# Optimization experiments

Hardware: AMD Instinct MI355X
Metric: run time of the kernel (lower is better)

The kernel has to match this reference:

```python
import jax, jax.numpy as jnp
import numpy as np
from jax import lax

SR = 4096.0        # sample_rate_Hz
N_LAYERS = 4
N_STATE = 64       # state_dim
E = 2              # d_inner (expand=2, d_model=1)
K = 4              # depthwise conv kernel
DT_RANK = 1
B, L = 32, 4096


def setup_inputs() -> dict:
    key = jax.random.key(0)
    ks = jax.random.split(key, 10)
    s = 0.02
    x = jax.random.normal(ks[0], (B, L), dtype=jnp.float32)
    W_in   = jax.random.normal(ks[1], (N_LAYERS, 1, 2 * E), jnp.float32) * 1.0
    conv_w = jax.random.normal(ks[2], (N_LAYERS, E, K), jnp.float32) * 0.5
    conv_b = jnp.zeros((N_LAYERS, E), jnp.float32)
    W_x    = jax.random.normal(ks[3], (N_LAYERS, E, DT_RANK + 2 * N_STATE), jnp.float32) * s
    W_dt   = jax.random.normal(ks[4], (N_LAYERS, DT_RANK, E), jnp.float32) * s
    b_dt   = jnp.zeros((N_LAYERS, E), jnp.float32)
    # S4D-real style init: A = -exp(A_log), A_log = log(1..N)
    A_log  = jnp.broadcast_to(jnp.log(jnp.arange(1, N_STATE + 1, dtype=jnp.float32)), (N_LAYERS, E, N_STATE)).copy()
    D_skip = jnp.ones((N_LAYERS, E), jnp.float32)
    W_out  = jax.random.normal(ks[5], (N_LAYERS, E, 1), jnp.float32) * s
    return {"x": x, "W_in": W_in, "conv_w": conv_w, "conv_b": conv_b, "W_x": W_x,
            "W_dt": W_dt, "b_dt": b_dt, "A_log": A_log, "D_skip": D_skip, "W_out": W_out}


def _causal_dwconv(u, w, b):
    # u: [B,L,E], w: [E,K] depthwise causal conv
    Klen = w.shape[1]
    up = jnp.pad(u, ((0, 0), (Klen - 1, 0), (0, 0)))
    y = sum(up[:, k:k + u.shape[1], :] * w[None, None, :, k] for k in range(Klen))
    return y + b


def _selective_scan(u, delta, A, Bm, Cm, Dv):
    # u,delta: [B,L,E]; A: [E,N]; Bm,Cm: [B,L,N]; Dv: [E]
    dA = jnp.exp(delta[..., None] * A)                       # [B,L,E,N]
    dBu = delta[..., None] * Bm[:, :, None, :] * u[..., None]  # [B,L,E,N]

    def step(h, inp):
        dA_t, dBu_t, C_t = inp                               # [B,E,N],[B,E,N],[B,N]
        h = dA_t * h + dBu_t
        y = jnp.einsum('ben,bn->be', h, C_t)
        return h, y

    h0 = jnp.zeros((u.shape[0],) + A.shape, dtype=u.dtype)
    _, ys = lax.scan(step, h0, (dA.transpose(1, 0, 2, 3), dBu.transpose(1, 0, 2, 3), Cm.transpose(1, 0, 2)))
    return ys.transpose(1, 0, 2) + u * Dv                    # [B,L,E]


def _mamba_block(x, W_in, conv_w, conv_b, W_x, W_dt, b_dt, A_log, D_skip, W_out):
    # x: [B,L,1]
    xz = x @ W_in                                            # [B,L,2E]
    u, z = xz[..., :E], xz[..., E:]
    u = jax.nn.silu(_causal_dwconv(u, conv_w, conv_b))       # [B,L,E]
    proj = u @ W_x                                           # [B,L,DT_RANK+2N]
    dt = proj[..., :DT_RANK]
    Bm = proj[..., DT_RANK:DT_RANK + N_STATE]
    Cm = proj[..., DT_RANK + N_STATE:]
    delta = jax.nn.softplus(dt @ W_dt + b_dt) / SR           # [B,L,E], timestep tied to sample rate
    A = -jnp.exp(A_log)                                      # [E,N]
    y = _selective_scan(u, delta, A, Bm, Cm, D_skip)
    y = y * jax.nn.silu(z)
    return y @ W_out + x                                     # residual, [B,L,1]


def reference(x, W_in, conv_w, conv_b, W_x, W_dt, b_dt, A_log, D_skip, W_out):
    h = x[..., None]                                         # [B,L,1]
    for i in range(N_LAYERS):
        h = _mamba_block(h, W_in[i], conv_w[i], conv_b[i], W_x[i], W_dt[i],
                         b_dt[i], A_log[i], D_skip[i], W_out[i])
    return h[..., 0]
```

## Files before the change

kernel.cpp:

```cpp
#include <hip/hip_runtime.h>
#include <hip/hip_bf16.h>


constexpr int   Bsz = 32;
constexpr int   Lsz = 4096;
constexpr int   NC  = 32;
constexpr int   CL  = 128;
constexpr float SRinv = 1.0f / 4096.0f;

__device__ __forceinline__ float sigmoidf_(float v) {
    return 1.0f / (1.0f + __expf(-v));
}

__global__ __launch_bounds__(128) void k_chunk_scan(
    const float* __restrict__ xin,
    const float* __restrict__ W_in,
    const float* __restrict__ conv_w,
    const float* __restrict__ conv_b,
    const float* __restrict__ W_x,
    const float* __restrict__ W_dt,
    const float* __restrict__ b_dt,
    const float* __restrict__ A_log,
    float4* __restrict__ ud,
    float*  __restrict__ Pc,
    float*  __restrict__ Sc)
{
    const int c = blockIdx.x, b = blockIdx.y, tid = threadIdx.x;
    __shared__ float  xs[CL + 3];
    __shared__ float4 s_ud[CL];
    const int base = b * Lsz + c * CL;

    for (int i = tid; i < CL + 3; i += 128) {
        int l = c * CL + i - 3;
        xs[i] = (l >= 0) ? xin[b * Lsz + l] : 0.0f;
    }
    __syncthreads();

    {
        const int t = tid;
        float x0 = xs[t], x1 = xs[t + 1], x2 = xs[t + 2], x3 = xs[t + 3];
        float u[2];
        #pragma unroll
        for (int e = 0; e < 2; e++) {
            float v = W_in[e] * (x0 * conv_w[e * 4 + 0] + x1 * conv_w[e * 4 + 1] +
                                 x2 * conv_w[e * 4 + 2] + x3 * conv_w[e * 4 + 3]) +
                      conv_b[e];
            u[e] = v * sigmoidf_(v);
        }
        float dt = u[0] * W_x[0] + u[1] * W_x[129];
        float dl[2];
        #pragma unroll
        for (int e = 0; e < 2; e++) {
            float a = dt * W_dt[e] + b_dt[e];
            float sp = (a > 20.0f) ? a : log1pf(__expf(a));
            dl[e] = sp * SRinv;
        }
        float4 v4 = make_float4(u[0], u[1], dl[0], dl[1]);
        s_ud[t] = v4;
        ud[base + t] = v4;
    }
    __syncthreads();

    const int e = tid >> 6, n = tid & 63;
    const float Aen = -__expf(A_log[e * 64 + n]);
    const float wb0 = W_x[1 + n], wb1 = W_x[129 + 1 + n];
    float P = 1.0f, S = 0.0f;
    #pragma unroll 8
    for (int l = 0; l < CL; l++) {
        float4 v = s_ud[l];
        float ue = e ? v.y : v.x;
        float d  = e ? v.w : v.z;
        float Bn = v.x * wb0 + v.y * wb1;
        float dA = __expf(d * Aen);
        S = dA * S + (d * ue) * Bn;
        P *= dA;
    }
    const int idx = (b * NC + c) * 128 + tid;
    Pc[idx] = P;
    Sc[idx] = S;
}

__global__ __launch_bounds__(256) void k_combine(
    const float* __restrict__ Pc, const float* __restrict__ Sc,
    float* __restrict__ Hinit)
{
    const int idx = blockIdx.x * 256 + threadIdx.x;
    const int b = idx >> 7, en = idx & 127;
    float h = 0.0f;
    #pragma unroll
    for (int c = 0; c < NC; c++) {
        int o = (b * NC + c) * 128 + en;
        Hinit[o] = h;
        h = Pc[o] * h + Sc[o];
    }
}

__global__ __launch_bounds__(128) void k_output(
    const float* __restrict__ xin,
    const float4* __restrict__ ud,
    const float* __restrict__ Hinit,
    const float* __restrict__ W_in,
    const float* __restrict__ W_x,
    const float* __restrict__ A_log,
    const float* __restrict__ D_skip,
    const float* __restrict__ W_out,
    float* __restrict__ out)
{
    const int c = blockIdx.x, b = blockIdx.y, tid = threadIdx.x;
    constexpr int T = 64;
    __shared__ float4 s_ud[CL];
    __shared__ float  xs[CL];
    __shared__ float  ps[128 * 65];
    __shared__ float  ys[T * 2];
    const int base = b * Lsz + c * CL;

    s_ud[tid] = ud[base + tid];
    xs[tid]   = xin[base + tid];

    const int e = tid >> 6, n = tid & 63;
    const float Aen = -__expf(A_log[e * 64 + n]);
    const float wb0 = W_x[1 + n],  wb1 = W_x[129 + 1 + n];
    const float wc0 = W_x[65 + n], wc1 = W_x[129 + 65 + n];
    float h = Hinit[(b * NC + c) * 128 + tid];
    const float wz0 = W_in[2], wz1 = W_in[3];
    const float D0 = D_skip[0], D1 = D_skip[1];
    const float wo0 = W_out[0], wo1 = W_out[1];
    __syncthreads();

    for (int tile = 0; tile < CL / T; tile++) {
        #pragma unroll 8
        for (int t = 0; t < T; t++) {
            float4 v = s_ud[tile * T + t];
            float ue = e ? v.y : v.x;
            float d  = e ? v.w : v.z;
            float Bn = v.x * wb0 + v.y * wb1;
            float Cn = v.x * wc0 + v.y * wc1;
            float dA = __expf(d * Aen);
            h = dA * h + (d * ue) * Bn;
            ps[(t * 2 + e) * 65 + n] = h * Cn;
        }
        __syncthreads();
        {
            const int r = tid, t = r >> 1, re = r & 1;
            const float* row = &ps[r * 65];
            float a0 = 0, a1 = 0, a2 = 0, a3 = 0;
            #pragma unroll
            for (int j = 0; j < 64; j += 4) {
                a0 += row[j]; a1 += row[j + 1]; a2 += row[j + 2]; a3 += row[j + 3];
            }
            float4 v = s_ud[tile * T + t];
            float ue = re ? v.y : v.x;
            ys[r] = (a0 + a1) + (a2 + a3) + ue * (re ? D1 : D0);
        }
        __syncthreads();
        if (tid < T) {
            int l = tile * T + tid;
            float y0 = ys[tid * 2], y1 = ys[tid * 2 + 1];
            float xv = xs[l];
            float z0 = xv * wz0, z1 = xv * wz1;
            out[base + l] = y0 * (z0 * sigmoidf_(z0)) * wo0 +
                            y1 * (z1 * sigmoidf_(z1)) * wo1 + xv;
        }
        __syncthreads();
    }
}

extern "C" void kernel_launch(void* const* d_in, const int* in_sizes, int n_in,
                              void* d_out, int out_size, void* d_ws, size_t ws_size,
                              hipStream_t stream) {
    const float* x      = (const float*)d_in[0];
    const float* W_in   = (const float*)d_in[1];
    const float* conv_w = (const float*)d_in[2];
    const float* conv_b = (const float*)d_in[3];
    const float* W_x    = (const float*)d_in[4];
    const float* W_dt   = (const float*)d_in[5];
    const float* b_dt   = (const float*)d_in[6];
    const float* A_log  = (const float*)d_in[7];
    const float* D_skip = (const float*)d_in[8];
    const float* W_out  = (const float*)d_in[9];
    float* out = (float*)d_out;

    float* ws   = (float*)d_ws;
    float4* ud  = (float4*)ws;
    float* Pc   = ws + (size_t)Bsz * Lsz * 4;
    float* Sc   = Pc + (size_t)Bsz * NC * 128;
    float* Hi   = Sc + (size_t)Bsz * NC * 128;
    float* buf0 = Hi + (size_t)Bsz * NC * 128;
    float* buf1 = buf0 + (size_t)Bsz * Lsz;

    const float* cur = x;
    for (int i = 0; i < 4; i++) {
        float* o = (i == 3) ? out : ((i & 1) ? buf1 : buf0);
        k_chunk_scan<<<dim3(NC, Bsz), 128, 0, stream>>>(
            cur, W_in + i * 4, conv_w + i * 8, conv_b + i * 2,
            W_x + i * 258, W_dt + i * 2, b_dt + i * 2, A_log + i * 128,
            ud, Pc, Sc);
        k_combine<<<16, 256, 0, stream>>>(Pc, Sc, Hi);
        k_output<<<dim3(NC, Bsz), 128, 0, stream>>>(
            cur, ud, Hi, W_in + i * 4, W_x + i * 258,
            A_log + i * 128, D_skip + i * 2, W_out + i * 2, o);
        cur = o;
    }
}
```

Measured before the change: 161.8 us.

## Fold chunk combine into output kernel and halve chunk length

Removes the separate combine kernel: each output block recomputes its starting state by serially folding the packed (P,S) pairs of all preceding chunks. Chunk length drops from 128 to 64 (twice the blocks, shorter serial scans), the per-direction branches are split by e to avoid selects, and the partial-sum reduction is split across two threads per row. This cuts one launch per layer and shortens the dependent chains. In exchange, later chunks perform up to 63 dependent global loads to rebuild their initial state, and the last chunk skips the P/S scan.

New measurement: 214.9 us. +32.8%, slower.

```diff
diff --git a/kernel.cpp b/kernel.cpp
--- a/kernel.cpp
+++ b/kernel.cpp
@@ -4,15 +4,16 @@
 
 constexpr int   Bsz = 32;
 constexpr int   Lsz = 4096;
-constexpr int   NC  = 32;
-constexpr int   CL  = 128;
+constexpr int   NC  = 64;
+constexpr int   CL  = 64;
+constexpr int   T   = 32;
 constexpr float SRinv = 1.0f / 4096.0f;
 
 __device__ __forceinline__ float sigmoidf_(float v) {
     return 1.0f / (1.0f + __expf(-v));
 }
 
-__global__ __launch_bounds__(128) void k_chunk_scan(
+__global__ __launch_bounds__(128) void k_scanA(
     const float* __restrict__ xin,
     const float* __restrict__ W_in,
     const float* __restrict__ conv_w,
@@ -22,8 +23,7 @@
     const float* __restrict__ b_dt,
     const float* __restrict__ A_log,
     float4* __restrict__ ud,
-    float*  __restrict__ Pc,
-    float*  __restrict__ Sc)
+    float2* __restrict__ PS)
 {
     const int c = blockIdx.x, b = blockIdx.y, tid = threadIdx.x;
     __shared__ float  xs[CL + 3];
@@ -36,7 +36,7 @@
     }
     __syncthreads();
 
-    {
+    if (tid < CL) {
         const int t = tid;
         float x0 = xs[t], x1 = xs[t + 1], x2 = xs[t + 2], x3 = xs[t + 3];
         float u[2];
@@ -61,44 +61,38 @@
     }
     __syncthreads();
 
+    if (c == NC - 1) return;
+
     const int e = tid >> 6, n = tid & 63;
     const float Aen = -__expf(A_log[e * 64 + n]);
     const float wb0 = W_x[1 + n], wb1 = W_x[129 + 1 + n];
     float P = 1.0f, S = 0.0f;
-    #pragma unroll 8
-    for (int l = 0; l < CL; l++) {
-        float4 v = s_ud[l];
-        float ue = e ? v.y : v.x;
-        float d  = e ? v.w : v.z;
-        float Bn = v.x * wb0 + v.y * wb1;
-        float dA = __expf(d * Aen);
-        S = dA * S + (d * ue) * Bn;
-        P *= dA;
-    }
-    const int idx = (b * NC + c) * 128 + tid;
-    Pc[idx] = P;
-    Sc[idx] = S;
-}
-
-__global__ __launch_bounds__(256) void k_combine(
-    const float* __restrict__ Pc, const float* __restrict__ Sc,
-    float* __restrict__ Hinit)
-{
-    const int idx = blockIdx.x * 256 + threadIdx.x;
-    const int b = idx >> 7, en = idx & 127;
-    float h = 0.0f;
-    #pragma unroll
-    for (int c = 0; c < NC; c++) {
-        int o = (b * NC + c) * 128 + en;
-        Hinit[o] = h;
-        h = Pc[o] * h + Sc[o];
-    }
-}
-
-__global__ __launch_bounds__(128) void k_output(
+    if (e == 0) {
+        #pragma unroll 8
+        for (int l = 0; l < CL; l++) {
+            float4 v = s_ud[l];
+            float Bn = v.x * wb0 + v.y * wb1;
+            float dA = __expf(v.z * Aen);
+            S = dA * S + (v.z * v.x) * Bn;
+            P *= dA;
+        }
+    } else {
+        #pragma unroll 8
+        for (int l = 0; l < CL; l++) {
+            float4 v = s_ud[l];
+            float Bn = v.x * wb0 + v.y * wb1;
+            float dA = __expf(v.w * Aen);
+            S = dA * S + (v.w * v.y) * Bn;
+            P *= dA;
+        }
+    }
+    PS[(b * NC + c) * 128 + tid] = make_float2(P, S);
+}
+
+__global__ __launch_bounds__(128) void k_scanB(
     const float* __restrict__ xin,
     const float4* __restrict__ ud,
-    const float* __restrict__ Hinit,
+    const float2* __restrict__ PS,
     const float* __restrict__ W_in,
     const float* __restrict__ W_x,
     const float* __restrict__ A_log,
@@ -107,55 +101,74 @@
     float* __restrict__ out)
 {
     const int c = blockIdx.x, b = blockIdx.y, tid = threadIdx.x;
-    constexpr int T = 64;
     __shared__ float4 s_ud[CL];
     __shared__ float  xs[CL];
-    __shared__ float  ps[128 * 65];
-    __shared__ float  ys[T * 2];
+    __shared__ float  ps[T * 2 * 65];
+    __shared__ float  pp[128];
     const int base = b * Lsz + c * CL;
 
-    s_ud[tid] = ud[base + tid];
-    xs[tid]   = xin[base + tid];
+    if (tid < CL) {
+        s_ud[tid] = ud[base + tid];
+        xs[tid]   = xin[base + tid];
+    }
+
+    float h = 0.0f;
+    {
+        const float2* p = &PS[(size_t)b * NC * 128 + tid];
+        for (int cp = 0; cp < c; cp++) {
+            float2 v = p[cp * 128];
+            h = v.x * h + v.y;
+        }
+    }
 
     const int e = tid >> 6, n = tid & 63;
     const float Aen = -__expf(A_log[e * 64 + n]);
     const float wb0 = W_x[1 + n],  wb1 = W_x[129 + 1 + n];
     const float wc0 = W_x[65 + n], wc1 = W_x[129 + 65 + n];
-    float h = Hinit[(b * NC + c) * 128 + tid];
     const float wz0 = W_in[2], wz1 = W_in[3];
     const float D0 = D_skip[0], D1 = D_skip[1];
     const float wo0 = W_out[0], wo1 = W_out[1];
     __syncthreads();
 
     for (int tile = 0; tile < CL / T; tile++) {
-        #pragma unroll 8
-        for (int t = 0; t < T; t++) {
-            float4 v = s_ud[tile * T + t];
-            float ue = e ? v.y : v.x;
-            float d  = e ? v.w : v.z;
-            float Bn = v.x * wb0 + v.y * wb1;
-            float Cn = v.x * wc0 + v.y * wc1;
-            float dA = __expf(d * Aen);
-            h = dA * h + (d * ue) * Bn;
-            ps[(t * 2 + e) * 65 + n] = h * Cn;
+        if (e == 0) {
+            #pragma unroll 8
+            for (int t = 0; t < T; t++) {
+                float4 v = s_ud[tile * T + t];
+                float Bn = v.x * wb0 + v.y * wb1;
+                float Cn = v.x * wc0 + v.y * wc1;
+                float dA = __expf(v.z * Aen);
+                h = dA * h + (v.z * v.x) * Bn;
+                ps[(t * 2 + 0) * 65 + n] = h * Cn;
+            }
+        } else {
+            #pragma unroll 8
+            for (int t = 0; t < T; t++) {
+                float4 v = s_ud[tile * T + t];
+                float Bn = v.x * wb0 + v.y * wb1;
+                float Cn = v.x * wc0 + v.y * wc1;
+                float dA = __expf(v.w * Aen);
+                h = dA * h + (v.w * v.y) * Bn;
+                ps[(t * 2 + 1) * 65 + n] = h * Cn;
+            }
         }
         __syncthreads();
         {
-            const int r = tid, t = r >> 1, re = r & 1;
-            const float* row = &ps[r * 65];
+            const int r = tid >> 1, half = tid & 1;
+            const float* row = &ps[r * 65 + half * 32];
             float a0 = 0, a1 = 0, a2 = 0, a3 = 0;
             #pragma unroll
-            for (int j = 0; j < 64; j += 4) {
+            for (int j = 0; j < 32; j += 4) {
                 a0 += row[j]; a1 += row[j + 1]; a2 += row[j + 2]; a3 += row[j + 3];
             }
-            float4 v = s_ud[tile * T + t];
-            float ue = re ? v.y : v.x;
-            ys[r] = (a0 + a1) + (a2 + a3) + ue * (re ? D1 : D0);
+            pp[tid] = (a0 + a1) + (a2 + a3);
         }
         __syncthreads();
         if (tid < T) {
             int l = tile * T + tid;
-            float y0 = ys[tid * 2], y1 = ys[tid * 2 + 1];
+            float4 v = s_ud[l];
+            float y0 = pp[tid * 4 + 0] + pp[tid * 4 + 1] + v.x * D0;
+            float y1 = pp[tid * 4 + 2] + pp[tid * 4 + 3] + v.y * D1;
             float xv = xs[l];
             float z0 = xv * wz0, z1 = xv * wz1;
             out[base + l] = y0 * (z0 * sigmoidf_(z0)) * wo0 +
@@ -180,24 +193,21 @@
     const float* W_out  = (const float*)d_in[9];
     float* out = (float*)d_out;
 
-    float* ws   = (float*)d_ws;
-    float4* ud  = (float4*)ws;
-    float* Pc   = ws + (size_t)Bsz * Lsz * 4;
-    float* Sc   = Pc + (size_t)Bsz * NC * 128;
-    float* Hi   = Sc + (size_t)Bsz * NC * 128;
-    float* buf0 = Hi + (size_t)Bsz * NC * 128;
-    float* buf1 = buf0 + (size_t)Bsz * Lsz;
+    float* ws    = (float*)d_ws;
+    float4* ud   = (float4*)ws;
+    float2* PS   = (float2*)(ws + (size_t)Bsz * Lsz * 4);
+    float*  buf0 = ws + (size_t)Bsz * Lsz * 4 + (size_t)Bsz * NC * 128 * 2;
+    float*  buf1 = buf0 + (size_t)Bsz * Lsz;
 
     const float* cur = x;
     for (int i = 0; i < 4; i++) {
         float* o = (i == 3) ? out : ((i & 1) ? buf1 : buf0);
-        k_chunk_scan<<<dim3(NC, Bsz), 128, 0, stream>>>(
+        k_scanA<<<dim3(NC, Bsz), 128, 0, stream>>>(
             cur, W_in + i * 4, conv_w + i * 8, conv_b + i * 2,
             W_x + i * 258, W_dt + i * 2, b_dt + i * 2, A_log + i * 128,
-            ud, Pc, Sc);
-        k_combine<<<16, 256, 0, stream>>>(Pc, Sc, Hi);
-        k_output<<<dim3(NC, Bsz), 128, 0, stream>>>(
-            cur, ud, Hi, W_in + i * 4, W_x + i * 258,
+            ud, PS);
+        k_scanB<<<dim3(NC, Bsz), 128, 0, stream>>>(
+            cur, ud, PS, W_in + i * 4, W_x + i * 258,
             A_log + i * 128, D_skip + i * 2, W_out + i * 2, o);
         cur = o;
     }
```
